# Kernel optimization log

Hardware: AMD Instinct MI355X
Metric: run time of the kernel (lower is better)

## Reference

```python
import jax, jax.numpy as jnp
import numpy as np

E = 512      # embed_dim
H = 8        # num_heads
D = E // H   # head_dim = 64
R = 32       # rot_dims (partial rotary)
THETA = 10000.0


def _rope(x):
    # x: [B, H, S, D]; rotate first R dims (interleaved pairs, lucidrains-style)
    S = x.shape[-2]
    inv_freq = THETA ** (-jnp.arange(0, R, 2, dtype=jnp.float32) / R)  # [R/2]
    ang = jnp.arange(S, dtype=jnp.float32)[:, None] * inv_freq          # [S, R/2]
    c, s = jnp.cos(ang), jnp.sin(ang)
    xr, xp = x[..., :R], x[..., R:]
    x1, x2 = xr[..., 0::2], xr[..., 1::2]
    rot = jnp.stack([x1 * c - x2 * s, x1 * s + x2 * c], axis=-1).reshape(xr.shape)
    return jnp.concatenate([rot, xp], axis=-1)


def setup_inputs() -> dict:
    key = jax.random.key(0)
    k1, k2, k3, k4 = jax.random.split(key, 4)
    B, S = 4, 2048
    x = jax.random.normal(k1, (B, S, E), dtype=jnp.float32)
    input_mask = jax.random.randint(k2, (B, S), 0, 2).astype(bool)
    W_in = jax.random.normal(k3, (3 * E, E), dtype=jnp.float32) / np.sqrt(E).astype(np.float32)
    W_out = jax.random.normal(k4, (E, E), dtype=jnp.float32) / np.sqrt(E).astype(np.float32)
    return {"x": x, "input_mask": input_mask, "W_in": W_in, "W_out": W_out}


def reference(x, input_mask, W_in, W_out):
    B, S, _ = x.shape
    # fused QKV projection (Linear, no bias): x @ W_in.T -> [B,S,3E]
    qkv = (x @ W_in.T).reshape(B, S, 3, H, D).transpose(2, 0, 3, 1, 4)  # [3,B,H,S,D]
    q, k, v = qkv[0], qkv[1], qkv[2]
    q = _rope(q)
    k = _rope(k)
    # mask: causal AND (both tokens valid OR diagonal)
    causal = jnp.tril(jnp.ones((S, S), dtype=bool))
    inv = ~input_mask                                  # [B,S]
    cross = inv[:, None, :] | inv[:, :, None]          # [B,S,S]
    square = (~cross) | jnp.eye(S, dtype=bool)         # diagonal forced True
    full = causal[None, :, :] & square                 # [B,S,S]
    scores = jnp.einsum('bhsd,bhtd->bhst', q, k) / np.float32(np.sqrt(D))
    scores = jnp.where(full[:, None, :, :], scores, -jnp.inf)
    probs = jax.nn.softmax(scores, axis=-1)
    attn = jnp.einsum('bhst,bhtd->bhsd', probs, v)
    attn = attn.transpose(0, 2, 1, 3).reshape(B, S, E)
    return attn @ W_out.T
```

## Files before the change

### kernel.cpp

```cpp
#include <hip/hip_runtime.h>
#include <math.h>

#define B_ 4
#define S_ 2048
#define E_ 512
#define H_ 8
#define D_ 64

typedef short bf16x8 __attribute__((ext_vector_type(8)));
typedef float f32x4 __attribute__((ext_vector_type(4)));

__device__ inline short f2bf(float f) {
  union { float f; unsigned u; } v; v.f = f;
  unsigned r = v.u + 0x7FFF + ((v.u >> 16) & 1);
  return (short)(r >> 16);
}

__global__ __launch_bounds__(256) void cvt_bf16(const float* __restrict__ src,
                                                short* __restrict__ dst, int n4) {
  int i = blockIdx.x * 256 + threadIdx.x;
  if (i < n4) {
    float4 f = ((const float4*)src)[i];
    short4 o;
    o.x = f2bf(f.x); o.y = f2bf(f.y); o.z = f2bf(f.z); o.w = f2bf(f.w);
    ((short4*)dst)[i] = o;
  }
}

__global__ __launch_bounds__(256) void gemm_qkv_mfma(
    const short* __restrict__ Xb,
    const short* __restrict__ Wb,
    short* __restrict__ qb, short* __restrict__ kb, short* __restrict__ vbT) {
  __shared__ __align__(16) short As[128][40];
  __shared__ __align__(16) short Bs[128][40];
  const int tid = threadIdx.x;
  const int w = tid >> 6, lane = tid & 63;
  const int l15 = lane & 15, quad = lane >> 4;
  const int wm = w & 1, wn = w >> 1;
  const int m0 = blockIdx.x * 128;
  const int n0 = blockIdx.y * 128;
  f32x4 acc[4][4];
  for (int mt = 0; mt < 4; ++mt)
    for (int nt = 0; nt < 4; ++nt) acc[mt][nt] = (f32x4){0.f, 0.f, 0.f, 0.f};

  for (int k0 = 0; k0 < E_; k0 += 32) {
    __syncthreads();
    for (int l = 0; l < 2; ++l) {
      int c = tid + 256 * l;
      int row = c >> 2, k8 = (c & 3) * 8;
      *(bf16x8*)&As[row][k8] = *(const bf16x8*)&Xb[(size_t)(m0 + row) * E_ + k0 + k8];
      *(bf16x8*)&Bs[row][k8] = *(const bf16x8*)&Wb[(size_t)(n0 + row) * E_ + k0 + k8];
    }
    __syncthreads();
    bf16x8 a[4], bfr[4];
    for (int mt = 0; mt < 4; ++mt)
      a[mt] = *(const bf16x8*)&As[wm * 64 + mt * 16 + l15][quad * 8];
    for (int nt = 0; nt < 4; ++nt)
      bfr[nt] = *(const bf16x8*)&Bs[wn * 64 + nt * 16 + l15][quad * 8];
    for (int mt = 0; mt < 4; ++mt)
      for (int nt = 0; nt < 4; ++nt)
        acc[mt][nt] = __builtin_amdgcn_mfma_f32_16x16x32_bf16(a[mt], bfr[nt], acc[mt][nt], 0, 0, 0);
  }
  const int t3 = n0 >> 9;
  for (int nt = 0; nt < 4; ++nt) {
    const int n = n0 + wn * 64 + nt * 16 + l15;
    const int h = (n >> 6) & 7;
    const int d = n & 63;
    const bool dorope = (t3 < 2) && (d < 32);
    const float sgn = (d & 1) ? 1.f : -1.f;
    const float fr = dorope ? powf(10000.f, -(float)(2 * (d >> 1)) * (1.f / 32.f)) : 0.f;
    for (int mt = 0; mt < 4; ++mt) {
      for (int i = 0; i < 4; ++i) {
        const int m = m0 + wm * 64 + mt * 16 + quad * 4 + i;
        const int b = m >> 11, s = m & (S_ - 1);
        float val = acc[mt][nt][i];
        float pv = __shfl_xor(val, 1, 64);
        float outv = val;
        if (dorope) {
          float ang = (float)s * fr;
          float sn, cs;
          sincosf(ang, &sn, &cs);
          outv = val * cs + pv * sgn * sn;
        }
        if (t3 == 2)
          vbT[((size_t)(b * 8 + h) * D_ + d) * S_ + s] = f2bf(outv);
        else {
          short* dst = (t3 == 0) ? qb : kb;
          dst[(((size_t)(b * 8 + h)) * S_ + s) * D_ + d] = f2bf(outv);
        }
      }
    }
  }
}

__global__ __launch_bounds__(256) void gemm_out_mfma(
    const short* __restrict__ Ab, const short* __restrict__ Wb,
    float* __restrict__ out) {
  __shared__ __align__(16) short As[128][40];
  __shared__ __align__(16) short Bs[128][40];
  const int tid = threadIdx.x;
  const int w = tid >> 6, lane = tid & 63;
  const int l15 = lane & 15, quad = lane >> 4;
  const int wm = w & 1, wn = w >> 1;
  const int m0 = blockIdx.x * 128;
  const int n0 = blockIdx.y * 128;
  f32x4 acc[4][4];
  for (int mt = 0; mt < 4; ++mt)
    for (int nt = 0; nt < 4; ++nt) acc[mt][nt] = (f32x4){0.f, 0.f, 0.f, 0.f};

  for (int k0 = 0; k0 < E_; k0 += 32) {
    __syncthreads();
    for (int l = 0; l < 2; ++l) {
      int c = tid + 256 * l;
      int row = c >> 2, k8 = (c & 3) * 8;
      *(bf16x8*)&As[row][k8] = *(const bf16x8*)&Ab[(size_t)(m0 + row) * E_ + k0 + k8];
      *(bf16x8*)&Bs[row][k8] = *(const bf16x8*)&Wb[(size_t)(n0 + row) * E_ + k0 + k8];
    }
    __syncthreads();
    bf16x8 a[4], bfr[4];
    for (int mt = 0; mt < 4; ++mt)
      a[mt] = *(const bf16x8*)&As[wm * 64 + mt * 16 + l15][quad * 8];
    for (int nt = 0; nt < 4; ++nt)
      bfr[nt] = *(const bf16x8*)&Bs[wn * 64 + nt * 16 + l15][quad * 8];
    for (int mt = 0; mt < 4; ++mt)
      for (int nt = 0; nt < 4; ++nt)
        acc[mt][nt] = __builtin_amdgcn_mfma_f32_16x16x32_bf16(a[mt], bfr[nt], acc[mt][nt], 0, 0, 0);
  }
  for (int mt = 0; mt < 4; ++mt)
    for (int nt = 0; nt < 4; ++nt) {
      const int n = n0 + wn * 64 + nt * 16 + l15;
      for (int i = 0; i < 4; ++i) {
        const int m = m0 + wm * 64 + mt * 16 + quad * 4 + i;
        out[(size_t)m * E_ + n] = acc[mt][nt][i];
      }
    }
}

__global__ __launch_bounds__(256) void flash_mfma(
    const short* __restrict__ qb, const short* __restrict__ kb,
    const short* __restrict__ vbT, const int* __restrict__ maskp,
    short* __restrict__ ob) {
  __shared__ __align__(16) short Ks[64][72];
  __shared__ __align__(16) short VT[64][72];
  __shared__ __align__(16) short Pl[4][16][72];
  __shared__ float kmf[64];
  const int tid = threadIdx.x;
  const int w = tid >> 6, lane = tid & 63;
  const int l15 = lane & 15, quad = lane >> 4;
  const int bh = blockIdx.y, b = bh >> 3, h = bh & 7;
  const short* qbase = qb + (size_t)bh * S_ * D_;
  const short* kbase = kb + (size_t)bh * S_ * D_;
  const short* vtb   = vbT + (size_t)bh * D_ * S_;
  bf16x8 ones;
  for (int j = 0; j < 8; ++j) ones[j] = (short)0x3F80;

  for (int seg = 0; seg < 2; ++seg) {
    const int r0 = (seg == 0) ? blockIdx.x * 64 : (S_ - 64) - blockIdx.x * 64;
    bf16x8 aq[2];
    {
      const short* qrow = qbase + (size_t)(r0 + 16 * w + l15) * D_;
      aq[0] = *(const bf16x8*)&qrow[quad * 8];
      aq[1] = *(const bf16x8*)&qrow[32 + quad * 8];
    }
    f32x4 o[4], lsum;
    for (int no = 0; no < 4; ++no) o[no] = (f32x4){0.f, 0.f, 0.f, 0.f};
    lsum = (f32x4){0.f, 0.f, 0.f, 0.f};

    const int lastkt = r0 >> 6;
    for (int kt = 0; kt <= lastkt; ++kt) {
      const int t0 = kt * 64;
      __syncthreads();
      for (int l = 0; l < 2; ++l) {
        int idx = tid + 256 * l;
        int row = idx >> 3, ch = (idx & 7) * 8;
        *(bf16x8*)&Ks[row][ch] = *(const bf16x8*)(kbase + (size_t)(t0 + row) * D_ + ch);
        *(bf16x8*)&VT[row][ch] = *(const bf16x8*)(vtb + (size_t)row * S_ + t0 + ch);
      }
      if (tid < 64) kmf[tid] = maskp[b * S_ + t0 + tid] ? 1.f : 0.f;
      __syncthreads();
      f32x4 sfr[4];
      for (int nb = 0; nb < 4; ++nb) sfr[nb] = (f32x4){0.f, 0.f, 0.f, 0.f};
      for (int nb = 0; nb < 4; ++nb)
        for (int ks = 0; ks < 2; ++ks) {
          bf16x8 bk = *(const bf16x8*)&Ks[l15 + 16 * nb][32 * ks + quad * 8];
          sfr[nb] = __builtin_amdgcn_mfma_f32_16x16x32_bf16(aq[ks], bk, sfr[nb], 0, 0, 0);
        }
      const bool boundary = (kt == lastkt);
      for (int nb = 0; nb < 4; ++nb) {
        const float km = kmf[l15 + 16 * nb];
        const int tg = l15 + 16 * nb;
        for (int i = 0; i < 4; ++i) {
          float pm = km;
          if (boundary && tg > 16 * w + quad * 4 + i) pm = 0.f;
          float p = __expf(sfr[nb][i] * 0.125f - 16.f) * pm;
          Pl[w][quad * 4 + i][l15 + 16 * nb] = f2bf(p);
        }
      }
      asm volatile("s_waitcnt lgkmcnt(0)" ::: "memory");
      bf16x8 ap0 = *(const bf16x8*)&Pl[w][l15][quad * 8];
      bf16x8 ap1 = *(const bf16x8*)&Pl[w][l15][32 + quad * 8];
      for (int no = 0; no < 4; ++no) {
        bf16x8 bv0 = *(const bf16x8*)&VT[16 * no + l15][quad * 8];
        bf16x8 bv1 = *(const bf16x8*)&VT[16 * no + l15][32 + quad * 8];
        o[no] = __builtin_amdgcn_mfma_f32_16x16x32_bf16(ap0, bv0, o[no], 0, 0, 0);
        o[no] = __builtin_amdgcn_mfma_f32_16x16x32_bf16(ap1, bv1, o[no], 0, 0, 0);
      }
      lsum = __builtin_amdgcn_mfma_f32_16x16x32_bf16(ap0, ones, lsum, 0, 0, 0);
      lsum = __builtin_amdgcn_mfma_f32_16x16x32_bf16(ap1, ones, lsum, 0, 0, 0);
    }
    for (int i = 0; i < 4; ++i) {
      const int s = r0 + 16 * w + quad * 4 + i;
      const int qm = maskp[b * S_ + s];
      const float inv = 1.f / lsum[i];
      short* orow = ob + ((size_t)(b * S_ + s)) * E_ + h * D_;
      for (int no = 0; no < 4; ++no) {
        const int d = l15 + 16 * no;
        orow[d] = qm ? f2bf(o[no][i] * inv) : vtb[(size_t)d * S_ + s];
      }
    }
  }
}

extern "C" void kernel_launch(void* const* d_in, const int* in_sizes, int n_in,
                              void* d_out, int out_size, void* d_ws, size_t ws_size,
                              hipStream_t stream) {
  const float* x    = (const float*)d_in[0];
  const int*   mask = (const int*)d_in[1];
  const float* Win  = (const float*)d_in[2];
  const float* Wout = (const float*)d_in[3];
  float* out = (float*)d_out;

  short* Xb    = (short*)d_ws;
  short* Winb  = Xb + 8192 * 512;
  short* Woutb = Winb + 1536 * 512;
  short* qb    = Woutb + 512 * 512;
  short* kb    = qb + 32 * 2048 * 64;
  short* vbT   = kb + 32 * 2048 * 64;
  short* ob    = vbT + 32 * 2048 * 64;

  cvt_bf16<<<4096, 256, 0, stream>>>(x, Xb, 8192 * 512 / 4);
  cvt_bf16<<<768, 256, 0, stream>>>(Win, Winb, 1536 * 512 / 4);
  cvt_bf16<<<256, 256, 0, stream>>>(Wout, Woutb, 512 * 512 / 4);
  gemm_qkv_mfma<<<dim3(64, 12), 256, 0, stream>>>(Xb, Winb, qb, kb, vbT);
  flash_mfma<<<dim3(16, 32), 256, 0, stream>>>(qb, kb, vbT, mask, ob);
  gemm_out_mfma<<<dim3(64, 4), 256, 0, stream>>>(ob, Woutb, out);
}
```

Measured before the change: 198.0 us.

## Split paired causal query tiles into separate blocks and fold mask into exp2 bias

The flash kernel no longer pairs a short and a long query tile inside one block. It launches one block per 64-row query tile (32x32 grid) and swizzles tile order per head and batch to spread causal work across CUs. The softmax numerator now uses exp2f with a pre-scaled constant and an additive key-mask bias instead of exp plus a multiply. It also uses a truncating-style fast bf16 rounding for P, and the diagonal-tile masking moves into a separate branch. This doubles the block count and relies on the hardware scheduler for load balance, and the rounding change slightly alters numerics.

New measurement: 209.1 us. 1.06x slower.

```diff
diff --git a/kernel.cpp b/kernel.cpp
--- a/kernel.cpp
+++ b/kernel.cpp
@@ -14,6 +14,10 @@
   union { float f; unsigned u; } v; v.f = f;
   unsigned r = v.u + 0x7FFF + ((v.u >> 16) & 1);
   return (short)(r >> 16);
+}
+__device__ inline short f2bf_fast(float f) {
+  union { float f; unsigned u; } v; v.f = f;
+  return (short)((v.u + 0x8000u) >> 16);
 }
 
 __global__ __launch_bounds__(256) void cvt_bf16(const float* __restrict__ src,
@@ -143,80 +147,86 @@
   __shared__ __align__(16) short Ks[64][72];
   __shared__ __align__(16) short VT[64][72];
   __shared__ __align__(16) short Pl[4][16][72];
-  __shared__ float kmf[64];
+  __shared__ float kbias[64];
   const int tid = threadIdx.x;
   const int w = tid >> 6, lane = tid & 63;
   const int l15 = lane & 15, quad = lane >> 4;
   const int bh = blockIdx.y, b = bh >> 3, h = bh & 7;
+  int qtb = (blockIdx.x + ((bh & 7) << 2)) & 31;
+  const int qt = ((bh >> 3) & 1) ? 31 - qtb : qtb;
+  const int r0 = qt * 64;
   const short* qbase = qb + (size_t)bh * S_ * D_;
   const short* kbase = kb + (size_t)bh * S_ * D_;
   const short* vtb   = vbT + (size_t)bh * D_ * S_;
+  const float c2 = 0.1803368801f;
   bf16x8 ones;
   for (int j = 0; j < 8; ++j) ones[j] = (short)0x3F80;
 
-  for (int seg = 0; seg < 2; ++seg) {
-    const int r0 = (seg == 0) ? blockIdx.x * 64 : (S_ - 64) - blockIdx.x * 64;
-    bf16x8 aq[2];
-    {
-      const short* qrow = qbase + (size_t)(r0 + 16 * w + l15) * D_;
-      aq[0] = *(const bf16x8*)&qrow[quad * 8];
-      aq[1] = *(const bf16x8*)&qrow[32 + quad * 8];
-    }
-    f32x4 o[4], lsum;
-    for (int no = 0; no < 4; ++no) o[no] = (f32x4){0.f, 0.f, 0.f, 0.f};
-    lsum = (f32x4){0.f, 0.f, 0.f, 0.f};
-
-    const int lastkt = r0 >> 6;
-    for (int kt = 0; kt <= lastkt; ++kt) {
-      const int t0 = kt * 64;
-      __syncthreads();
-      for (int l = 0; l < 2; ++l) {
-        int idx = tid + 256 * l;
-        int row = idx >> 3, ch = (idx & 7) * 8;
-        *(bf16x8*)&Ks[row][ch] = *(const bf16x8*)(kbase + (size_t)(t0 + row) * D_ + ch);
-        *(bf16x8*)&VT[row][ch] = *(const bf16x8*)(vtb + (size_t)row * S_ + t0 + ch);
-      }
-      if (tid < 64) kmf[tid] = maskp[b * S_ + t0 + tid] ? 1.f : 0.f;
-      __syncthreads();
-      f32x4 sfr[4];
-      for (int nb = 0; nb < 4; ++nb) sfr[nb] = (f32x4){0.f, 0.f, 0.f, 0.f};
-      for (int nb = 0; nb < 4; ++nb)
-        for (int ks = 0; ks < 2; ++ks) {
-          bf16x8 bk = *(const bf16x8*)&Ks[l15 + 16 * nb][32 * ks + quad * 8];
-          sfr[nb] = __builtin_amdgcn_mfma_f32_16x16x32_bf16(aq[ks], bk, sfr[nb], 0, 0, 0);
+  bf16x8 aq[2];
+  {
+    const short* qrow = qbase + (size_t)(r0 + 16 * w + l15) * D_;
+    aq[0] = *(const bf16x8*)&qrow[quad * 8];
+    aq[1] = *(const bf16x8*)&qrow[32 + quad * 8];
+  }
+  f32x4 o[4], lsum;
+  for (int no = 0; no < 4; ++no) o[no] = (f32x4){0.f, 0.f, 0.f, 0.f};
+  lsum = (f32x4){0.f, 0.f, 0.f, 0.f};
+
+  for (int kt = 0; kt <= qt; ++kt) {
+    const int t0 = kt * 64;
+    __syncthreads();
+    for (int l = 0; l < 2; ++l) {
+      int idx = tid + 256 * l;
+      int row = idx >> 3, ch = (idx & 7) * 8;
+      *(bf16x8*)&Ks[row][ch] = *(const bf16x8*)(kbase + (size_t)(t0 + row) * D_ + ch);
+      *(bf16x8*)&VT[row][ch] = *(const bf16x8*)(vtb + (size_t)row * S_ + t0 + ch);
+    }
+    if (tid < 64)
+      kbias[tid] = maskp[b * S_ + t0 + tid] ? -23.08312f : -1.0e38f;
+    __syncthreads();
+    f32x4 sfr[4];
+    for (int nb = 0; nb < 4; ++nb) sfr[nb] = (f32x4){0.f, 0.f, 0.f, 0.f};
+    for (int nb = 0; nb < 4; ++nb)
+      for (int ks = 0; ks < 2; ++ks) {
+        bf16x8 bk = *(const bf16x8*)&Ks[l15 + 16 * nb][32 * ks + quad * 8];
+        sfr[nb] = __builtin_amdgcn_mfma_f32_16x16x32_bf16(aq[ks], bk, sfr[nb], 0, 0, 0);
+      }
+    if (kt < qt) {
+      for (int nb = 0; nb < 4; ++nb) {
+        const float bb = kbias[l15 + 16 * nb];
+        for (int i = 0; i < 4; ++i)
+          Pl[w][quad * 4 + i][l15 + 16 * nb] = f2bf_fast(exp2f(sfr[nb][i] * c2 + bb));
+      }
+    } else {
+      for (int nb = 0; nb < 4; ++nb) {
+        const int tg = l15 + 16 * nb;
+        const float bb = kbias[l15 + 16 * nb];
+        for (int i = 0; i < 4; ++i) {
+          const float bbi = (tg > 16 * w + quad * 4 + i) ? -1.0e38f : bb;
+          Pl[w][quad * 4 + i][l15 + 16 * nb] = f2bf_fast(exp2f(sfr[nb][i] * c2 + bbi));
         }
-      const bool boundary = (kt == lastkt);
-      for (int nb = 0; nb < 4; ++nb) {
-        const float km = kmf[l15 + 16 * nb];
-        const int tg = l15 + 16 * nb;
-        for (int i = 0; i < 4; ++i) {
-          float pm = km;
-          if (boundary && tg > 16 * w + quad * 4 + i) pm = 0.f;
-          float p = __expf(sfr[nb][i] * 0.125f - 16.f) * pm;
-          Pl[w][quad * 4 + i][l15 + 16 * nb] = f2bf(p);
-        }
-      }
-      asm volatile("s_waitcnt lgkmcnt(0)" ::: "memory");
-      bf16x8 ap0 = *(const bf16x8*)&Pl[w][l15][quad * 8];
-      bf16x8 ap1 = *(const bf16x8*)&Pl[w][l15][32 + quad * 8];
-      for (int no = 0; no < 4; ++no) {
-        bf16x8 bv0 = *(const bf16x8*)&VT[16 * no + l15][quad * 8];
-        bf16x8 bv1 = *(const bf16x8*)&VT[16 * no + l15][32 + quad * 8];
-        o[no] = __builtin_amdgcn_mfma_f32_16x16x32_bf16(ap0, bv0, o[no], 0, 0, 0);
-        o[no] = __builtin_amdgcn_mfma_f32_16x16x32_bf16(ap1, bv1, o[no], 0, 0, 0);
-      }
-      lsum = __builtin_amdgcn_mfma_f32_16x16x32_bf16(ap0, ones, lsum, 0, 0, 0);
-      lsum = __builtin_amdgcn_mfma_f32_16x16x32_bf16(ap1, ones, lsum, 0, 0, 0);
-    }
-    for (int i = 0; i < 4; ++i) {
-      const int s = r0 + 16 * w + quad * 4 + i;
-      const int qm = maskp[b * S_ + s];
-      const float inv = 1.f / lsum[i];
-      short* orow = ob + ((size_t)(b * S_ + s)) * E_ + h * D_;
-      for (int no = 0; no < 4; ++no) {
-        const int d = l15 + 16 * no;
-        orow[d] = qm ? f2bf(o[no][i] * inv) : vtb[(size_t)d * S_ + s];
-      }
+      }
+    }
+    asm volatile("s_waitcnt lgkmcnt(0)" ::: "memory");
+    bf16x8 ap0 = *(const bf16x8*)&Pl[w][l15][quad * 8];
+    bf16x8 ap1 = *(const bf16x8*)&Pl[w][l15][32 + quad * 8];
+    for (int no = 0; no < 4; ++no) {
+      bf16x8 bv0 = *(const bf16x8*)&VT[16 * no + l15][quad * 8];
+      bf16x8 bv1 = *(const bf16x8*)&VT[16 * no + l15][32 + quad * 8];
+      o[no] = __builtin_amdgcn_mfma_f32_16x16x32_bf16(ap0, bv0, o[no], 0, 0, 0);
+      o[no] = __builtin_amdgcn_mfma_f32_16x16x32_bf16(ap1, bv1, o[no], 0, 0, 0);
+    }
+    lsum = __builtin_amdgcn_mfma_f32_16x16x32_bf16(ap0, ones, lsum, 0, 0, 0);
+    lsum = __builtin_amdgcn_mfma_f32_16x16x32_bf16(ap1, ones, lsum, 0, 0, 0);
+  }
+  for (int i = 0; i < 4; ++i) {
+    const int s = r0 + 16 * w + quad * 4 + i;
+    const int qm = maskp[b * S_ + s];
+    const float inv = 1.f / lsum[i];
+    short* orow = ob + ((size_t)(b * S_ + s)) * E_ + h * D_;
+    for (int no = 0; no < 4; ++no) {
+      const int d = l15 + 16 * no;
+      orow[d] = qm ? f2bf(o[no][i] * inv) : vtb[(size_t)d * S_ + s];
     }
   }
 }
@@ -242,6 +252,6 @@
   cvt_bf16<<<768, 256, 0, stream>>>(Win, Winb, 1536 * 512 / 4);
   cvt_bf16<<<256, 256, 0, stream>>>(Wout, Woutb, 512 * 512 / 4);
   gemm_qkv_mfma<<<dim3(64, 12), 256, 0, stream>>>(Xb, Winb, qb, kb, vbT);
-  flash_mfma<<<dim3(16, 32), 256, 0, stream>>>(qb, kb, vbT, mask, ob);
+  flash_mfma<<<dim3(32, 32), 256, 0, stream>>>(qb, kb, vbT, mask, ob);
   gemm_out_mfma<<<dim3(64, 4), 256, 0, stream>>>(ob, Woutb, out);
 }
```
